# Optimization experiments

Hardware: AMD Instinct MI355X
Metric: run time of the kernel (lower is better)

Reference implementation:

```python
import jax, jax.numpy as jnp
import numpy as np

B, S, D, H = 2, 2048, 1024, 16
DK = D // H


def setup_inputs() -> dict:
    key = jax.random.key(0)
    ks = jax.random.split(key, 12)
    k_init = 1.0 / np.sqrt(D)  # torch Linear-style uniform bound used in the module
    def lin(kw, kb):
        W = jax.random.uniform(kw, (D, D), jnp.float32, -k_init, k_init)
        b = jax.random.uniform(kb, (D,), jnp.float32, -k_init, k_init)
        return W, b
    Wq, bq = lin(ks[0], ks[1])
    Wk, bk = lin(ks[2], ks[3])
    Wv, bv = lin(ks[4], ks[5])
    Wo, bo = lin(ks[6], ks[7])
    query = jax.random.normal(ks[8], (B, S, D), jnp.float32)
    key_t = jax.random.normal(ks[9], (B, S, D), jnp.float32)
    value = jax.random.normal(ks[10], (B, S, D), jnp.float32)
    # causal mask: 1 where attention allowed, 0 where blocked
    mask = jnp.broadcast_to(jnp.tril(jnp.ones((S, S), jnp.int32)), (B, S, S))
    return {"query": query, "key": key_t, "value": value, "mask": mask,
            "Wq": Wq, "bq": bq, "Wk": Wk, "bk": bk, "Wv": Wv, "bv": bv,
            "Wo": Wo, "bo": bo}


def reference(query, key, value, mask, Wq, bq, Wk, bk, Wv, bv, Wo, bo):
    bs = query.shape[0]
    # projections: torch Linear computes x @ W.T + b
    def proj(x, W, b):
        y = x @ W.T + b                      # [B, S, D]
        return y.reshape(bs, -1, H, DK).transpose(0, 2, 1, 3)  # [B, H, S, DK]
    q = proj(query, Wq, bq)
    k = proj(key, Wk, bk)
    v = proj(value, Wv, bv)
    scale = 1.0 / np.sqrt(DK).astype(np.float32)
    scores = jnp.einsum('bhqd,bhkd->bhqk', q, k) * scale  # [B, H, S, S]
    scores = jnp.where(mask[:, None, :, :] == 0, jnp.float32(-1e9), scores)
    p_attn = jax.nn.softmax(scores, axis=-1)
    # dropout omitted (eval mode / deterministic reference)
    x = jnp.einsum('bhqk,bhkd->bhqd', p_attn, v)          # [B, H, S, DK]
    x = x.transpose(0, 2, 1, 3).reshape(bs, -1, D)        # [B, S, D]
    return x @ Wo.T + bo
```

## Files before the change

kernel.cpp:

```cpp
#include <hip/hip_runtime.h>
#include <hip/hip_bf16.h>
#include <math.h>

#define BB 2
#define SS 2048
#define DD 1024
#define HH 16
#define DKK 64
#define NT (BB * SS)
#define QBLK 128
#define NQT (SS / QBLK)

typedef __attribute__((ext_vector_type(8))) short short8;
typedef __attribute__((ext_vector_type(4))) float f32x4;

#define SWZ(r) ((((r) >> 3) ^ (r)) & 7)

__device__ __forceinline__ unsigned short f2b(float x) {
    __hip_bfloat16 h = __float2bfloat16(x);
    unsigned short u; __builtin_memcpy(&u, &h, 2); return u;
}

__device__ __forceinline__ f32x4 zero4() {
    f32x4 z; z[0] = 0.f; z[1] = 0.f; z[2] = 0.f; z[3] = 0.f; return z;
}

template <typename AT, typename OutT>
__device__ __forceinline__ void gemm_body(const AT* __restrict__ A,
                                          const float* __restrict__ W,
                                          const float* __restrict__ bias,
                                          OutT* __restrict__ C,
                                          int bm, int bn, int N, int K) {
    __shared__ __align__(16) unsigned char sA[128 * 128];
    __shared__ __align__(16) unsigned char sB[128 * 128];

    const int tid = threadIdx.x;
    const int l = tid & 63;
    const int w = tid >> 6;
    const int wr = w >> 1, wc = w & 1;
    const int g = l >> 4, li = l & 15;

    f32x4 acc[4][4];
    #pragma unroll
    for (int i = 0; i < 4; ++i)
        #pragma unroll
        for (int jj = 0; jj < 4; ++jj) acc[i][jj] = zero4();

    for (int kt = 0; kt < K; kt += 64) {
        #pragma unroll
        for (int c = 0; c < 4; ++c) {
            const int ch = c * 256 + tid;
            const int row = ch >> 3, cj = ch & 7;
            short8 va, vb;
            if constexpr (sizeof(AT) == 4) {
                const float* p = (const float*)A + (size_t)(bm + row) * K + kt + cj * 8;
                const float4 a0 = *reinterpret_cast<const float4*>(p);
                const float4 a1 = *reinterpret_cast<const float4*>(p + 4);
                #pragma unroll
                for (int jj = 0; jj < 4; ++jj) {
                    va[jj]     = (short)f2b(((const float*)&a0)[jj]);
                    va[4 + jj] = (short)f2b(((const float*)&a1)[jj]);
                }
            } else {
                va = *reinterpret_cast<const short8*>(
                    (const unsigned short*)A + (size_t)(bm + row) * K + kt + cj * 8);
            }
            {
                const float* p = W + (size_t)(bn + row) * K + kt + cj * 8;
                const float4 b0 = *reinterpret_cast<const float4*>(p);
                const float4 b1 = *reinterpret_cast<const float4*>(p + 4);
                #pragma unroll
                for (int jj = 0; jj < 4; ++jj) {
                    vb[jj]     = (short)f2b(((const float*)&b0)[jj]);
                    vb[4 + jj] = (short)f2b(((const float*)&b1)[jj]);
                }
            }
            *reinterpret_cast<short8*>(&sA[row * 128 + ((cj ^ SWZ(row)) << 4)]) = va;
            *reinterpret_cast<short8*>(&sB[row * 128 + ((cj ^ SWZ(row)) << 4)]) = vb;
        }
        __syncthreads();

        #pragma unroll
        for (int kb = 0; kb < 2; ++kb) {
            short8 af[4], bfr[4];
            const int ch = g + kb * 4;
            #pragma unroll
            for (int mi = 0; mi < 4; ++mi) {
                const int row = wr * 64 + mi * 16 + li;
                af[mi] = *reinterpret_cast<const short8*>(&sA[row * 128 + ((ch ^ SWZ(row)) << 4)]);
            }
            #pragma unroll
            for (int ni = 0; ni < 4; ++ni) {
                const int row = wc * 64 + ni * 16 + li;
                bfr[ni] = *reinterpret_cast<const short8*>(&sB[row * 128 + ((ch ^ SWZ(row)) << 4)]);
            }
            #pragma unroll
            for (int mi = 0; mi < 4; ++mi)
                #pragma unroll
                for (int ni = 0; ni < 4; ++ni)
                    acc[mi][ni] = __builtin_amdgcn_mfma_f32_16x16x32_bf16(af[mi], bfr[ni], acc[mi][ni], 0, 0, 0);
        }
        __syncthreads();
    }

    #pragma unroll
    for (int ni = 0; ni < 4; ++ni) {
        const int col = bn + wc * 64 + ni * 16 + li;
        const float bv = bias[col];
        #pragma unroll
        for (int mi = 0; mi < 4; ++mi) {
            const int row0 = bm + wr * 64 + mi * 16 + g * 4;
            #pragma unroll
            for (int r = 0; r < 4; ++r) {
                const float v = acc[mi][ni][r] + bv;
                if constexpr (sizeof(OutT) == 2)
                    C[(size_t)(row0 + r) * N + col] = (OutT)f2b(v);
                else
                    C[(size_t)(row0 + r) * N + col] = (OutT)v;
            }
        }
    }
}

struct QKVArgs {
    const float* A[3];
    const float* W[3];
    const float* bias[3];
    unsigned short* C[3];
};

__global__ __launch_bounds__(256)
void gemm_qkv(QKVArgs args) {
    const int bid = blockIdx.x;
    const int i = (bid & 7) * 96 + (bid >> 3);
    const int z = i >> 8;
    const int rem = i & 255;
    const int by = rem >> 3, bx = rem & 7;
    gemm_body<float, unsigned short>(args.A[z], args.W[z], args.bias[z], args.C[z],
                                     by * 128, bx * 128, DD, DD);
}

__global__ __launch_bounds__(256)
void gemm_out(const unsigned short* __restrict__ A, const float* __restrict__ W,
              const float* __restrict__ bias, float* __restrict__ C) {
    const int bid = blockIdx.x;
    const int i = (bid & 7) * 32 + (bid >> 3);
    const int by = i >> 3, bx = i & 7;
    gemm_body<unsigned short, float>(A, W, bias, C, by * 128, bx * 128, DD, DD);
}

__global__ __launch_bounds__(512)
void attn_mfma(const unsigned short* __restrict__ Q,
               const unsigned short* __restrict__ Kb,
               const unsigned short* __restrict__ Vb,
               unsigned short* __restrict__ X) {
    __shared__ __align__(16) unsigned char sK[64 * 128];
    __shared__ __align__(16) unsigned char sV[64 * 128];
    __shared__ __align__(16) unsigned char sP[8][16 * 128];

    const int bid = blockIdx.x;
    const int j = bid >> 3;
    const int pair = (bid & 7) * 4 + (j >> 4);
    const int qt = (NQT - 1) - (j & 15);
    const int b = pair >> 4, h = pair & 15;

    const int tid = threadIdx.x, l = tid & 63, w = tid >> 6;
    const int g = l >> 4, li = l & 15;
    const int tok0 = b * SS + qt * QBLK;
    const int col0 = h * DKK;
    const float scale = 0.125f;

    short8 qf[2];
    {
        const size_t qrow = (size_t)(tok0 + w * 16 + li) * DD + col0;
        qf[0] = *reinterpret_cast<const short8*>(&Q[qrow + g * 8]);
        qf[1] = *reinterpret_cast<const short8*>(&Q[qrow + 32 + g * 8]);
    }

    f32x4 accO[4];
    #pragma unroll
    for (int i = 0; i < 4; ++i) accO[i] = zero4();
    float m = -INFINITY, lsum = 0.f;
    const int qglob = qt * QBLK + w * 16 + li;
    const int qminw = qt * QBLK + w * 16;
    const int ktmax = 2 * qt + 1;

    for (int kt = 0; kt <= ktmax; ++kt) {
        const int ktok0 = b * SS + kt * 64;

        {
            const int row = tid >> 3, cj = tid & 7;
            const size_t gsrc = (size_t)(ktok0 + row) * DD + col0 + cj * 8;
            const short8 kv8 = *reinterpret_cast<const short8*>(&Kb[gsrc]);
            *reinterpret_cast<short8*>(&sK[row * 128 + ((cj ^ SWZ(row)) << 4)]) = kv8;
            const short8 vv8 = *reinterpret_cast<const short8*>(&Vb[gsrc]);
            #pragma unroll
            for (int jj = 0; jj < 8; ++jj) {
                const int d = cj * 8 + jj;
                *reinterpret_cast<unsigned short*>(
                    &sV[d * 128 + (((row >> 3) ^ SWZ(d)) << 4) + (row & 7) * 2]) =
                    (unsigned short)vv8[jj];
            }
        }
        __syncthreads();

        if (kt * 64 <= qminw + 15) {
            f32x4 accS[4];
            #pragma unroll
            for (int n0 = 0; n0 < 4; ++n0) accS[n0] = zero4();
            #pragma unroll
            for (int n0 = 0; n0 < 4; ++n0) {
                #pragma unroll
                for (int kb = 0; kb < 2; ++kb) {
                    const int row = n0 * 16 + li;
                    const int ch = g + kb * 4;
                    const short8 kf = *reinterpret_cast<const short8*>(
                        &sK[row * 128 + ((ch ^ SWZ(row)) << 4)]);
                    accS[n0] = __builtin_amdgcn_mfma_f32_16x16x32_bf16(kf, qf[kb], accS[n0], 0, 0, 0);
                }
            }

            const bool needMask = (kt * 64 + 63) > qminw;
            float s[16];
            float tmax = -INFINITY;
            #pragma unroll
            for (int n0 = 0; n0 < 4; ++n0)
                #pragma unroll
                for (int r = 0; r < 4; ++r) {
                    float v = accS[n0][r] * scale;
                    if (needMask) {
                        const int kv = kt * 64 + n0 * 16 + g * 4 + r;
                        if (kv > qglob) v = -1e30f;
                    }
                    s[n0 * 4 + r] = v;
                    tmax = fmaxf(tmax, v);
                }
            tmax = fmaxf(tmax, __shfl_xor(tmax, 16));
            tmax = fmaxf(tmax, __shfl_xor(tmax, 32));
            const float mnew = fmaxf(m, tmax);
            const float corr = __expf(m - mnew);
            float psum = 0.f;
            #pragma unroll
            for (int i = 0; i < 16; ++i) { s[i] = __expf(s[i] - mnew); psum += s[i]; }
            psum += __shfl_xor(psum, 16);
            psum += __shfl_xor(psum, 32);
            lsum = lsum * corr + psum;
            m = mnew;

            #pragma unroll
            for (int n0 = 0; n0 < 4; ++n0)
                #pragma unroll
                for (int r = 0; r < 4; ++r) {
                    const int kv = n0 * 16 + g * 4 + r;
                    *reinterpret_cast<unsigned short*>(
                        &sP[w][li * 128 + (((kv >> 3) ^ SWZ(li)) << 4) + (kv & 7) * 2]) =
                        f2b(s[n0 * 4 + r]);
                }

            float corr4[4];
            #pragma unroll
            for (int r = 0; r < 4; ++r) corr4[r] = __shfl(corr, (l & 48) | (g * 4 + r));
            #pragma unroll
            for (int n0d = 0; n0d < 4; ++n0d)
                #pragma unroll
                for (int r = 0; r < 4; ++r) accO[n0d][r] *= corr4[r];

            #pragma unroll
            for (int kb = 0; kb < 2; ++kb) {
                const int ch = g + kb * 4;
                const short8 pf = *reinterpret_cast<const short8*>(
                    &sP[w][li * 128 + ((ch ^ SWZ(li)) << 4)]);
                #pragma unroll
                for (int n0d = 0; n0d < 4; ++n0d) {
                    const int d = n0d * 16 + li;
                    const short8 vf = *reinterpret_cast<const short8*>(
                        &sV[d * 128 + ((ch ^ SWZ(d)) << 4)]);
                    accO[n0d] = __builtin_amdgcn_mfma_f32_16x16x32_bf16(pf, vf, accO[n0d], 0, 0, 0);
                }
            }
        }
        __syncthreads();
    }

    const float invl = 1.f / lsum;
    float inv4[4];
    #pragma unroll
    for (int r = 0; r < 4; ++r) inv4[r] = __shfl(invl, (l & 48) | (g * 4 + r));
    #pragma unroll
    for (int n0d = 0; n0d < 4; ++n0d)
        #pragma unroll
        for (int r = 0; r < 4; ++r) {
            const int row = tok0 + w * 16 + g * 4 + r;
            const int d = n0d * 16 + li;
            X[(size_t)row * DD + col0 + d] = f2b(accO[n0d][r] * inv4[r]);
        }
}

extern "C" void kernel_launch(void* const* d_in, const int* in_sizes, int n_in,
                              void* d_out, int out_size, void* d_ws, size_t ws_size,
                              hipStream_t stream) {
    const float* query = (const float*)d_in[0];
    const float* key   = (const float*)d_in[1];
    const float* value = (const float*)d_in[2];
    const float* Wq = (const float*)d_in[4];
    const float* bq = (const float*)d_in[5];
    const float* Wk = (const float*)d_in[6];
    const float* bk = (const float*)d_in[7];
    const float* Wv = (const float*)d_in[8];
    const float* bv = (const float*)d_in[9];
    const float* Wo = (const float*)d_in[10];
    const float* bo = (const float*)d_in[11];
    float* out = (float*)d_out;

    unsigned short* ws16 = (unsigned short*)d_ws;
    const size_t TOK = (size_t)NT * DD;
    unsigned short* qb = ws16;
    unsigned short* kb = ws16 + TOK;
    unsigned short* vb = ws16 + 2 * TOK;
    unsigned short* xb = ws16 + 3 * TOK;

    QKVArgs args;
    args.A[0] = query; args.A[1] = key; args.A[2] = value;
    args.W[0] = Wq;    args.W[1] = Wk;  args.W[2] = Wv;
    args.bias[0] = bq; args.bias[1] = bk; args.bias[2] = bv;
    args.C[0] = qb;    args.C[1] = kb;  args.C[2] = vb;

    gemm_qkv<<<768, 256, 0, stream>>>(args);
    attn_mfma<<<512, 512, 0, stream>>>(qb, kb, vb, xb);
    gemm_out<<<256, 256, 0, stream>>>(xb, Wo, bo, out);
}
```

Baseline: 316.7 us.

## Pre-cast inputs and weights to bf16 and load GEMM tiles directly into LDS

Adds a single cast kernel that converts query/key/value and all four weight matrices to bf16 in workspace. The GEMMs then load bf16 tiles via global_load_lds straight into shared memory, with no in-register conversion. This is meant to cut repeated fp32 reads and conversion work inside the GEMM loops. In exchange it adds an extra full pass over the inputs, and it drops the LDS swizzle, which may introduce bank conflicts on the fragment reads.

```diff
diff --git a/kernel.cpp b/kernel.cpp
--- a/kernel.cpp
+++ b/kernel.cpp
@@ -25,9 +25,32 @@
     f32x4 z; z[0] = 0.f; z[1] = 0.f; z[2] = 0.f; z[3] = 0.f; return z;
 }
 
-template <typename AT, typename OutT>
-__device__ __forceinline__ void gemm_body(const AT* __restrict__ A,
-                                          const float* __restrict__ W,
+struct CastAll {
+    const float* src[7];
+    unsigned short* dst[7];
+};
+
+__global__ __launch_bounds__(256)
+void cast_all(CastAll a) {
+    const int tid0 = blockIdx.x * 256 + threadIdx.x;
+    const int stride = gridDim.x * 256;
+    #pragma unroll
+    for (int s = 0; s < 7; ++s) {
+        const int n4 = (s < 3) ? (NT * DD / 4) : (DD * DD / 4);
+        const float* __restrict__ src = a.src[s];
+        unsigned short* __restrict__ dst = a.dst[s];
+        for (int i = tid0; i < n4; i += stride) {
+            const float4 v = reinterpret_cast<const float4*>(src)[i];
+            ushort4 o;
+            o.x = f2b(v.x); o.y = f2b(v.y); o.z = f2b(v.z); o.w = f2b(v.w);
+            reinterpret_cast<ushort4*>(dst)[i] = o;
+        }
+    }
+}
+
+template <typename OutT>
+__device__ __forceinline__ void gemm_body(const unsigned short* __restrict__ A,
+                                          const unsigned short* __restrict__ W,
                                           const float* __restrict__ bias,
                                           OutT* __restrict__ C,
                                           int bm, int bn, int N, int K) {
@@ -39,6 +62,8 @@
     const int w = tid >> 6;
     const int wr = w >> 1, wc = w & 1;
     const int g = l >> 4, li = l & 15;
+    const int lrow = l >> 3;
+    const int lcol = (l & 7) * 8;
 
     f32x4 acc[4][4];
     #pragma unroll
@@ -49,51 +74,32 @@
     for (int kt = 0; kt < K; kt += 64) {
         #pragma unroll
         for (int c = 0; c < 4; ++c) {
-            const int ch = c * 256 + tid;
-            const int row = ch >> 3, cj = ch & 7;
-            short8 va, vb;
-            if constexpr (sizeof(AT) == 4) {
-                const float* p = (const float*)A + (size_t)(bm + row) * K + kt + cj * 8;
-                const float4 a0 = *reinterpret_cast<const float4*>(p);
-                const float4 a1 = *reinterpret_cast<const float4*>(p + 4);
-                #pragma unroll
-                for (int jj = 0; jj < 4; ++jj) {
-                    va[jj]     = (short)f2b(((const float*)&a0)[jj]);
-                    va[4 + jj] = (short)f2b(((const float*)&a1)[jj]);
-                }
-            } else {
-                va = *reinterpret_cast<const short8*>(
-                    (const unsigned short*)A + (size_t)(bm + row) * K + kt + cj * 8);
-            }
-            {
-                const float* p = W + (size_t)(bn + row) * K + kt + cj * 8;
-                const float4 b0 = *reinterpret_cast<const float4*>(p);
-                const float4 b1 = *reinterpret_cast<const float4*>(p + 4);
-                #pragma unroll
-                for (int jj = 0; jj < 4; ++jj) {
-                    vb[jj]     = (short)f2b(((const float*)&b0)[jj]);
-                    vb[4 + jj] = (short)f2b(((const float*)&b1)[jj]);
-                }
-            }
-            *reinterpret_cast<short8*>(&sA[row * 128 + ((cj ^ SWZ(row)) << 4)]) = va;
-            *reinterpret_cast<short8*>(&sB[row * 128 + ((cj ^ SWZ(row)) << 4)]) = vb;
+            const int row0 = w * 32 + c * 8;
+            const unsigned short* gA = A + (size_t)(bm + row0 + lrow) * K + kt + lcol;
+            __builtin_amdgcn_global_load_lds(
+                (const __attribute__((address_space(1))) unsigned int*)gA,
+                (__attribute__((address_space(3))) unsigned int*)&sA[row0 * 128],
+                16, 0, 0);
+            const unsigned short* gB = W + (size_t)(bn + row0 + lrow) * K + kt + lcol;
+            __builtin_amdgcn_global_load_lds(
+                (const __attribute__((address_space(1))) unsigned int*)gB,
+                (__attribute__((address_space(3))) unsigned int*)&sB[row0 * 128],
+                16, 0, 0);
         }
         __syncthreads();
 
         #pragma unroll
         for (int kb = 0; kb < 2; ++kb) {
+            const int chb = (g + kb * 4) * 16;
             short8 af[4], bfr[4];
-            const int ch = g + kb * 4;
-            #pragma unroll
-            for (int mi = 0; mi < 4; ++mi) {
-                const int row = wr * 64 + mi * 16 + li;
-                af[mi] = *reinterpret_cast<const short8*>(&sA[row * 128 + ((ch ^ SWZ(row)) << 4)]);
-            }
-            #pragma unroll
-            for (int ni = 0; ni < 4; ++ni) {
-                const int row = wc * 64 + ni * 16 + li;
-                bfr[ni] = *reinterpret_cast<const short8*>(&sB[row * 128 + ((ch ^ SWZ(row)) << 4)]);
-            }
+            #pragma unroll
+            for (int mi = 0; mi < 4; ++mi)
+                af[mi] = *reinterpret_cast<const short8*>(
+                    &sA[(wr * 64 + mi * 16 + li) * 128 + chb]);
+            #pragma unroll
+            for (int ni = 0; ni < 4; ++ni)
+                bfr[ni] = *reinterpret_cast<const short8*>(
+                    &sB[(wc * 64 + ni * 16 + li) * 128 + chb]);
             #pragma unroll
             for (int mi = 0; mi < 4; ++mi)
                 #pragma unroll
@@ -123,8 +129,8 @@
 }
 
 struct QKVArgs {
-    const float* A[3];
-    const float* W[3];
+    const unsigned short* A[3];
+    const unsigned short* W[3];
     const float* bias[3];
     unsigned short* C[3];
 };
@@ -136,17 +142,17 @@
     const int z = i >> 8;
     const int rem = i & 255;
     const int by = rem >> 3, bx = rem & 7;
-    gemm_body<float, unsigned short>(args.A[z], args.W[z], args.bias[z], args.C[z],
-                                     by * 128, bx * 128, DD, DD);
+    gemm_body<unsigned short>(args.A[z], args.W[z], args.bias[z], args.C[z],
+                              by * 128, bx * 128, DD, DD);
 }
 
 __global__ __launch_bounds__(256)
-void gemm_out(const unsigned short* __restrict__ A, const float* __restrict__ W,
+void gemm_out(const unsigned short* __restrict__ A, const unsigned short* __restrict__ W,
               const float* __restrict__ bias, float* __restrict__ C) {
     const int bid = blockIdx.x;
     const int i = (bid & 7) * 32 + (bid >> 3);
     const int by = i >> 3, bx = i & 7;
-    gemm_body<unsigned short, float>(A, W, bias, C, by * 128, bx * 128, DD, DD);
+    gemm_body<float>(A, W, bias, C, by * 128, bx * 128, DD, DD);
 }
 
 __global__ __launch_bounds__(512)
@@ -314,18 +320,37 @@
 
     unsigned short* ws16 = (unsigned short*)d_ws;
     const size_t TOK = (size_t)NT * DD;
-    unsigned short* qb = ws16;
-    unsigned short* kb = ws16 + TOK;
-    unsigned short* vb = ws16 + 2 * TOK;
-    unsigned short* xb = ws16 + 3 * TOK;
+    const size_t WSZ = (size_t)DD * DD;
+    unsigned short* qb  = ws16;
+    unsigned short* kb  = ws16 + TOK;
+    unsigned short* vb  = ws16 + 2 * TOK;
+    unsigned short* xb  = ws16 + 3 * TOK;
+    unsigned short* xqb = ws16 + 4 * TOK;
+    unsigned short* xkb = ws16 + 5 * TOK;
+    unsigned short* xvb = ws16 + 6 * TOK;
+    unsigned short* wqb = ws16 + 7 * TOK;
+    unsigned short* wkb = wqb + WSZ;
+    unsigned short* wvb = wkb + WSZ;
+    unsigned short* wob = wvb + WSZ;
+
+    CastAll ca;
+    ca.src[0] = query; ca.dst[0] = xqb;
+    ca.src[1] = key;   ca.dst[1] = xkb;
+    ca.src[2] = value; ca.dst[2] = xvb;
+    ca.src[3] = Wq;    ca.dst[3] = wqb;
+    ca.src[4] = Wk;    ca.dst[4] = wkb;
+    ca.src[5] = Wv;    ca.dst[5] = wvb;
+    ca.src[6] = Wo;    ca.dst[6] = wob;
+    cast_all<<<2048, 256, 0, stream>>>(ca);
 
     QKVArgs args;
-    args.A[0] = query; args.A[1] = key; args.A[2] = value;
-    args.W[0] = Wq;    args.W[1] = Wk;  args.W[2] = Wv;
+    args.A[0] = xqb; args.A[1] = xkb; args.A[2] = xvb;
+    args.W[0] = wqb; args.W[1] = wkb; args.W[2] = wvb;
     args.bias[0] = bq; args.bias[1] = bk; args.bias[2] = bv;
-    args.C[0] = qb;    args.C[1] = kb;  args.C[2] = vb;
-
+    args.C[0] = qb;  args.C[1] = kb;  args.C[2] = vb;
     gemm_qkv<<<768, 256, 0, stream>>>(args);
+
     attn_mfma<<<512, 512, 0, stream>>>(qb, kb, vb, xb);
-    gemm_out<<<256, 256, 0, stream>>>(xb, Wo, bo, out);
-}
+
+    gemm_out<<<256, 256, 0, stream>>>(xb, wob, bo, out);
+}
```

New measurement: 291.0 us. -8.1%, faster.
